# Optimization experiments

Hardware: AMD Instinct MI355X
Metric: run time of the kernel (lower is better)

The kernel has to match this reference:

```python
import jax, jax.numpy as jnp
import numpy as np

B, S, D, H = 2, 48, 256, 8
DH = D // H  # depth per head = 32
N = S * S    # flattened pair sequence length = 2304


def setup_inputs() -> dict:
    key = jax.random.key(0)
    ks = jax.random.split(key, 9)
    std = 1.0 / np.sqrt(D)
    x = jax.random.normal(ks[0], (B, S, S, D), dtype=jnp.float32)
    Wq = jax.random.normal(ks[1], (D, D), dtype=jnp.float32) * std
    Wk = jax.random.normal(ks[2], (D, D), dtype=jnp.float32) * std
    Wv = jax.random.normal(ks[3], (D, D), dtype=jnp.float32) * std
    Wo = jax.random.normal(ks[4], (D, D), dtype=jnp.float32) * std
    bq = jnp.zeros((D,), jnp.float32)
    bk = jnp.zeros((D,), jnp.float32)
    bv = jnp.zeros((D,), jnp.float32)
    bo = jnp.zeros((D,), jnp.float32)
    return {"pair_representation": x, "Wq": Wq, "bq": bq, "Wk": Wk, "bk": bk,
            "Wv": Wv, "bv": bv, "Wo": Wo, "bo": bo}


def reference(pair_representation, Wq, bq, Wk, bk, Wv, bv, Wo, bo):
    x = pair_representation.reshape(B, N, D)  # flatten (S,S) -> N

    def heads(t):  # (B,N,D) -> (B,H,N,DH)
        return t.reshape(B, N, H, DH).transpose(0, 2, 1, 3)

    q = heads(x @ Wq + bq)
    k = heads(x @ Wk + bk)
    v = heads(x @ Wv + bv)

    scale = 1.0 / jnp.sqrt(jnp.asarray(DH, jnp.float32))
    logits = jnp.einsum('bhnd,bhmd->bhnm', q, k) * scale  # (B,H,N,N)
    attn = jax.nn.softmax(logits, axis=-1)
    ctx = jnp.einsum('bhnm,bhmd->bhnd', attn, v)
    ctx = ctx.transpose(0, 2, 1, 3).reshape(B, N, D)
    return ctx @ Wo + bo  # (B, N, D)
```

## Files before the change

kernel.cpp:

```cpp
#include <hip/hip_runtime.h>
#include <math.h>

#define B 2
#define S 48
#define D 256
#define H 8
#define DH 32
#define N (S*S)
#define BN (B*N)
#define BH (B*H)
#define KS 4
#define KPZ (N/KS)
#define NE ((size_t)BN*D)
#define BHN (BH*N)

typedef _Float16 half8 __attribute__((ext_vector_type(8)));
typedef _Float16 half4_t __attribute__((ext_vector_type(4)));
typedef unsigned short ushort8_t __attribute__((ext_vector_type(8)));
typedef float floatx4 __attribute__((ext_vector_type(4)));

__device__ __forceinline__ void split8(const float* v, half8* hi, half8* lo) {
    #pragma unroll
    for (int j = 0; j < 8; j++) {
        _Float16 h = (_Float16)v[j];
        (*hi)[j] = h;
        (*lo)[j] = (_Float16)(v[j] - (float)h);
    }
}

__global__ __launch_bounds__(256) void convert_w(
    const float* __restrict__ Wq, const float* __restrict__ Wk,
    const float* __restrict__ Wv, const float* __restrict__ Wo,
    _Float16* __restrict__ wqh, _Float16* __restrict__ wql,
    _Float16* __restrict__ wkh, _Float16* __restrict__ wkl,
    _Float16* __restrict__ wvh, _Float16* __restrict__ wvl,
    _Float16* __restrict__ woh, _Float16* __restrict__ wol)
{
    const int t = threadIdx.x;
    const int z = blockIdx.y;
    const int tr = blockIdx.x >> 2, tc = blockIdx.x & 3;
    const float* W = (z == 0) ? Wq : (z == 1) ? Wk : (z == 2) ? Wv : Wo;
    _Float16* oh   = (z == 0) ? wqh : (z == 1) ? wkh : (z == 2) ? wvh : woh;
    _Float16* ol   = (z == 0) ? wql : (z == 1) ? wkl : (z == 2) ? wvl : wol;

    __shared__ float Ws[64 * 68];
    #pragma unroll
    for (int i = 0; i < 4; i++) {
        int idx = i * 1024 + t * 4;
        int r = idx >> 6, c = idx & 63;
        *(float4*)(&Ws[r * 68 + c]) =
            *(const float4*)(W + (size_t)(tr * 64 + r) * D + tc * 64 + c);
    }
    __syncthreads();
    #pragma unroll
    for (int it = 0; it < 2; it++) {
        int idx = it * 256 + t;
        int cc = idx & 63, k0 = (idx >> 6) * 8;
        float v[8];
        #pragma unroll
        for (int j = 0; j < 8; j++) v[j] = Ws[(k0 + j) * 68 + cc];
        half8 hi, lo;
        split8(v, &hi, &lo);
        size_t ob = (size_t)(tc * 64 + cc) * D + tr * 64 + k0;
        *(half8*)(oh + ob) = hi;
        *(half8*)(ol + ob) = lo;
    }
}

__global__ __launch_bounds__(256) void proj_gemm(
    const float* __restrict__ x,
    const _Float16* __restrict__ wqh, const _Float16* __restrict__ wql,
    const _Float16* __restrict__ wkh, const _Float16* __restrict__ wkl,
    const _Float16* __restrict__ wvh, const _Float16* __restrict__ wvl,
    const float* __restrict__ bq, const float* __restrict__ bk,
    const float* __restrict__ bv,
    _Float16* __restrict__ qh_o, _Float16* __restrict__ ql_o,
    _Float16* __restrict__ kh_o, _Float16* __restrict__ kl_o,
    _Float16* __restrict__ vh_o)
{
    __shared__ __align__(16) _Float16 AhS[64 * 72];
    __shared__ __align__(16) _Float16 AlS[64 * 72];
    __shared__ __align__(16) _Float16 BhS[64 * 72];
    __shared__ __align__(16) _Float16 BlS[64 * 72];

    const int z = blockIdx.z;
    const _Float16* bth = (z == 0) ? wqh : (z == 1) ? wkh : wvh;
    const _Float16* btl = (z == 0) ? wql : (z == 1) ? wkl : wvl;
    const float* bias   = (z == 0) ? bq : (z == 1) ? bk : bv;
    _Float16* oh        = (z == 0) ? qh_o : (z == 1) ? kh_o : vh_o;
    _Float16* ol        = (z == 0) ? ql_o : kl_o;
    const float scale   = (z == 0) ? rsqrtf((float)DH) * 1.44269504f : 1.0f;

    const int t = threadIdx.x;
    const int wv2 = t >> 6, lane = t & 63, l15 = lane & 15, quad = lane >> 4;
    const int rowbase = blockIdx.x * 64;
    const int colbase = blockIdx.y * 64;
    floatx4 acc[4] = {{0,0,0,0},{0,0,0,0},{0,0,0,0},{0,0,0,0}};

    for (int kb = 0; kb < D; kb += 64) {
        __syncthreads();
        #pragma unroll
        for (int i = 0; i < 2; i++) {
            int idx = i * 2048 + t * 8;
            int r = idx >> 6, c = idx & 63;
            const float* xp = x + (size_t)(rowbase + r) * D + kb + c;
            float4 x0 = *(const float4*)xp;
            float4 x1 = *(const float4*)(xp + 4);
            float v[8] = {x0.x, x0.y, x0.z, x0.w, x1.x, x1.y, x1.z, x1.w};
            half8 hi, lo;
            split8(v, &hi, &lo);
            *(half8*)(AhS + r * 72 + c) = hi;
            *(half8*)(AlS + r * 72 + c) = lo;
            *(ushort8_t*)(BhS + r * 72 + c) =
                *(const ushort8_t*)(bth + (size_t)(colbase + r) * D + kb + c);
            *(ushort8_t*)(BlS + r * 72 + c) =
                *(const ushort8_t*)(btl + (size_t)(colbase + r) * D + kb + c);
        }
        __syncthreads();
        #pragma unroll
        for (int ksx = 0; ksx < 2; ksx++) {
            half8 ah = *(const half8*)(AhS + (wv2 * 16 + l15) * 72 + ksx * 32 + quad * 8);
            half8 al = *(const half8*)(AlS + (wv2 * 16 + l15) * 72 + ksx * 32 + quad * 8);
            #pragma unroll
            for (int cg = 0; cg < 4; cg++) {
                half8 bh8 = *(const half8*)(BhS + (cg * 16 + l15) * 72 + ksx * 32 + quad * 8);
                half8 bl8 = *(const half8*)(BlS + (cg * 16 + l15) * 72 + ksx * 32 + quad * 8);
                acc[cg] = __builtin_amdgcn_mfma_f32_16x16x32_f16(ah, bh8, acc[cg], 0, 0, 0);
                acc[cg] = __builtin_amdgcn_mfma_f32_16x16x32_f16(al, bh8, acc[cg], 0, 0, 0);
                acc[cg] = __builtin_amdgcn_mfma_f32_16x16x32_f16(ah, bl8, acc[cg], 0, 0, 0);
            }
        }
    }

    const int bb = (rowbase >= N) ? 1 : 0;
    #pragma unroll
    for (int cg = 0; cg < 4; cg++) {
        int col = colbase + cg * 16 + l15;
        int hh = col >> 5, dh = col & 31;
        float bs = bias[col];
        #pragma unroll
        for (int r = 0; r < 4; r++) {
            int n = rowbase + wv2 * 16 + quad * 4 + r - bb * N;
            float v = (acc[cg][r] + bs) * scale;
            size_t ob = ((size_t)(bb * H + hh) * N + n) * DH + dh;
            _Float16 hi = (_Float16)v;
            oh[ob] = hi;
            if (z < 2) ol[ob] = (_Float16)(v - (float)hi);
        }
    }
}

__global__ __launch_bounds__(256) void attn_kernel(
    const _Float16* __restrict__ qh, const _Float16* __restrict__ ql,
    const _Float16* __restrict__ kh, const _Float16* __restrict__ kl,
    const _Float16* __restrict__ vh,
    float* __restrict__ ctx_part, float* __restrict__ lpart)
{
    __shared__ __align__(16) _Float16 Kh[64 * 40];
    __shared__ __align__(16) _Float16 Kl[64 * 40];
    __shared__ __align__(16) _Float16 Vt[32 * 72];

    const int t = threadIdx.x;
    const int wv2 = t >> 6, lane = t & 63, l15 = lane & 15, quad = lane >> 4;
    const int bh = blockIdx.y, kz = blockIdx.z;
    const int qbase = blockIdx.x * 128 + wv2 * 32;

    half4_t bqh[2][2], bql[2][2];
    #pragma unroll
    for (int qg = 0; qg < 2; qg++) {
        const size_t qoff = ((size_t)bh * N + qbase + qg * 16 + l15) * DH + quad * 4;
        bqh[qg][0] = *(const half4_t*)(qh + qoff);
        bqh[qg][1] = *(const half4_t*)(qh + qoff + 16);
        bql[qg][0] = *(const half4_t*)(ql + qoff);
        bql[qg][1] = *(const half4_t*)(ql + qoff + 16);
    }

    floatx4 acc[2][2] = {{{0,0,0,0},{0,0,0,0}},{{0,0,0,0},{0,0,0,0}}};
    float lsum[2] = {0.f, 0.f};

    const _Float16* kh_g = kh + (size_t)bh * N * DH;
    const _Float16* kl_g = kl + (size_t)bh * N * DH;
    const _Float16* vh_g = vh + (size_t)bh * N * DH;

    const int skey = t >> 2;
    const int sd0  = (t & 3) * 8;
    const int srot = 2 * (t & 3);

    for (int it = 0; it < KPZ / 64; it++) {
        const int key0 = kz * KPZ + it * 64;
        __syncthreads();
        {
            const size_t g = (size_t)key0 * DH + t * 8;
            ushort8_t kv = *(const ushort8_t*)(kh_g + g);
            ushort8_t lv = *(const ushort8_t*)(kl_g + g);
            ushort8_t vv = *(const ushort8_t*)(vh_g + g);
            *(ushort8_t*)(Kh + skey * 40 + sd0) = kv;
            *(ushort8_t*)(Kl + skey * 40 + sd0) = lv;
            unsigned short* vt = (unsigned short*)Vt;
            #pragma unroll
            for (int j = 0; j < 8; j++) {
                int jj = (j + srot) & 7;
                vt[(sd0 + jj) * 72 + skey] = vv[jj];
            }
        }
        __syncthreads();

        #pragma unroll
        for (int kg = 0; kg < 4; kg++) {
            const _Float16* kr = Kh + (kg * 16 + l15) * 40 + quad * 4;
            const _Float16* lr = Kl + (kg * 16 + l15) * 40 + quad * 4;
            half4_t ah0 = *(const half4_t*)(kr);
            half4_t ah1 = *(const half4_t*)(kr + 16);
            half4_t al0 = *(const half4_t*)(lr);
            half4_t al1 = *(const half4_t*)(lr + 16);
            half4_t va0 = *(const half4_t*)(Vt + l15 * 72 + kg * 16 + quad * 4);
            half4_t va1 = *(const half4_t*)(Vt + (16 + l15) * 72 + kg * 16 + quad * 4);
            #pragma unroll
            for (int qg = 0; qg < 2; qg++) {
                floatx4 s = {0, 0, 0, 0};
                s = __builtin_amdgcn_mfma_f32_16x16x16f16(ah0, bqh[qg][0], s, 0, 0, 0);
                s = __builtin_amdgcn_mfma_f32_16x16x16f16(al0, bqh[qg][0], s, 0, 0, 0);
                s = __builtin_amdgcn_mfma_f32_16x16x16f16(ah0, bql[qg][0], s, 0, 0, 0);
                s = __builtin_amdgcn_mfma_f32_16x16x16f16(ah1, bqh[qg][1], s, 0, 0, 0);
                s = __builtin_amdgcn_mfma_f32_16x16x16f16(al1, bqh[qg][1], s, 0, 0, 0);
                s = __builtin_amdgcn_mfma_f32_16x16x16f16(ah1, bql[qg][1], s, 0, 0, 0);
                float p0 = exp2f(s[0]), p1 = exp2f(s[1]);
                float p2 = exp2f(s[2]), p3 = exp2f(s[3]);
                lsum[qg] += (p0 + p1) + (p2 + p3);
                half4_t pf;
                pf[0] = (_Float16)p0; pf[1] = (_Float16)p1;
                pf[2] = (_Float16)p2; pf[3] = (_Float16)p3;
                acc[qg][0] = __builtin_amdgcn_mfma_f32_16x16x16f16(va0, pf, acc[qg][0], 0, 0, 0);
                acc[qg][1] = __builtin_amdgcn_mfma_f32_16x16x16f16(va1, pf, acc[qg][1], 0, 0, 0);
            }
        }
    }

    const int bb = bh / H, hh = bh % H;
    float* cp = ctx_part + (size_t)kz * NE;
    float* lp = lpart + (size_t)kz * BHN;
    #pragma unroll
    for (int qg = 0; qg < 2; qg++) {
        float ls = lsum[qg];
        ls += __shfl_xor(ls, 16);
        ls += __shfl_xor(ls, 32);
        int q = qbase + qg * 16 + l15;
        if (quad == 0) lp[bh * N + q] = ls;
        float* crow = cp + ((size_t)bb * N + q) * D + hh * DH;
        #pragma unroll
        for (int dg = 0; dg < 2; dg++)
            #pragma unroll
            for (int r = 0; r < 4; r++)
                crow[dg * 16 + quad * 4 + r] = acc[qg][dg][r];
    }
}

__global__ __launch_bounds__(256) void outproj_gemm(
    const float* __restrict__ ctx_part, const float* __restrict__ lpart,
    const _Float16* __restrict__ woh, const _Float16* __restrict__ wol,
    const float* __restrict__ bo, float* __restrict__ out)
{
    __shared__ __align__(16) _Float16 AhS[64 * 72];
    __shared__ __align__(16) _Float16 AlS[64 * 72];
    __shared__ __align__(16) _Float16 BhS[64 * 72];
    __shared__ __align__(16) _Float16 BlS[64 * 72];

    const int t = threadIdx.x;
    const int wv2 = t >> 6, lane = t & 63, l15 = lane & 15, quad = lane >> 4;
    const int rowbase = blockIdx.x * 64;
    const int colbase = blockIdx.y * 64;
    floatx4 acc[4] = {{0,0,0,0},{0,0,0,0},{0,0,0,0},{0,0,0,0}};

    for (int kb = 0; kb < D; kb += 64) {
        __syncthreads();
        #pragma unroll
        for (int i = 0; i < 2; i++) {
            int idx = i * 2048 + t * 8;
            int r = idx >> 6, c = idx & 63;
            int row = rowbase + r;
            int kcol = kb + c;
            int bb = (row >= N) ? 1 : 0;
            int n = row - bb * N;
            int bhn = (bb * H + (kcol >> 5)) * N + n;
            float ls = lpart[bhn] + lpart[BHN + bhn]
                     + lpart[2 * BHN + bhn] + lpart[3 * BHN + bhn];
            float inv = 1.0f / ls;
            const float* pp = ctx_part + (size_t)row * D + kcol;
            float4 a0 = *(const float4*)(pp),          a1 = *(const float4*)(pp + 4);
            float4 b0 = *(const float4*)(pp + NE),     b1 = *(const float4*)(pp + NE + 4);
            float4 c0 = *(const float4*)(pp + 2 * NE), c1 = *(const float4*)(pp + 2 * NE + 4);
            float4 d0 = *(const float4*)(pp + 3 * NE), d1 = *(const float4*)(pp + 3 * NE + 4);
            float v[8] = {(a0.x + b0.x + c0.x + d0.x) * inv,
                          (a0.y + b0.y + c0.y + d0.y) * inv,
                          (a0.z + b0.z + c0.z + d0.z) * inv,
                          (a0.w + b0.w + c0.w + d0.w) * inv,
                          (a1.x + b1.x + c1.x + d1.x) * inv,
                          (a1.y + b1.y + c1.y + d1.y) * inv,
                          (a1.z + b1.z + c1.z + d1.z) * inv,
                          (a1.w + b1.w + c1.w + d1.w) * inv};
            half8 hi, lo;
            split8(v, &hi, &lo);
            *(half8*)(AhS + r * 72 + c) = hi;
            *(half8*)(AlS + r * 72 + c) = lo;
            *(ushort8_t*)(BhS + r * 72 + c) =
                *(const ushort8_t*)(woh + (size_t)(colbase + r) * D + kb + c);
            *(ushort8_t*)(BlS + r * 72 + c) =
                *(const ushort8_t*)(wol + (size_t)(colbase + r) * D + kb + c);
        }
        __syncthreads();
        #pragma unroll
        for (int ksx = 0; ksx < 2; ksx++) {
            half8 ah = *(const half8*)(AhS + (wv2 * 16 + l15) * 72 + ksx * 32 + quad * 8);
            half8 al = *(const half8*)(AlS + (wv2 * 16 + l15) * 72 + ksx * 32 + quad * 8);
            #pragma unroll
            for (int cg = 0; cg < 4; cg++) {
                half8 bh8 = *(const half8*)(BhS + (cg * 16 + l15) * 72 + ksx * 32 + quad * 8);
                half8 bl8 = *(const half8*)(BlS + (cg * 16 + l15) * 72 + ksx * 32 + quad * 8);
                acc[cg] = __builtin_amdgcn_mfma_f32_16x16x32_f16(ah, bh8, acc[cg], 0, 0, 0);
                acc[cg] = __builtin_amdgcn_mfma_f32_16x16x32_f16(al, bh8, acc[cg], 0, 0, 0);
                acc[cg] = __builtin_amdgcn_mfma_f32_16x16x32_f16(ah, bl8, acc[cg], 0, 0, 0);
            }
        }
    }

    #pragma unroll
    for (int cg = 0; cg < 4; cg++) {
        int col = colbase + cg * 16 + l15;
        float bs = bo[col];
        #pragma unroll
        for (int r = 0; r < 4; r++) {
            int row = rowbase + wv2 * 16 + quad * 4 + r;
            out[(size_t)row * D + col] = acc[cg][r] + bs;
        }
    }
}

extern "C" void kernel_launch(void* const* d_in, const int* in_sizes, int n_in,
                              void* d_out, int out_size, void* d_ws, size_t ws_size,
                              hipStream_t stream)
{
    const float* x  = (const float*)d_in[0];
    const float* Wq = (const float*)d_in[1];
    const float* bq = (const float*)d_in[2];
    const float* Wk = (const float*)d_in[3];
    const float* bk = (const float*)d_in[4];
    const float* Wv = (const float*)d_in[5];
    const float* bv = (const float*)d_in[6];
    const float* Wo = (const float*)d_in[7];
    const float* bo = (const float*)d_in[8];
    float* out = (float*)d_out;

    const size_t WE = (size_t)D * D;

    float* ctx_part = (float*)d_ws;
    float* lpart    = ctx_part + (size_t)KS * NE;
    _Float16* qh  = (_Float16*)(lpart + (size_t)KS * BHN);
    _Float16* ql  = qh + NE;
    _Float16* kh  = ql + NE;
    _Float16* kl  = kh + NE;
    _Float16* vh  = kl + NE;
    _Float16* wqh = vh + NE;
    _Float16* wql = wqh + WE;
    _Float16* wkh = wql + WE;
    _Float16* wkl = wkh + WE;
    _Float16* wvh = wkl + WE;
    _Float16* wvl = wvh + WE;
    _Float16* woh = wvl + WE;
    _Float16* wol = woh + WE;

    convert_w<<<dim3(16, 4), 256, 0, stream>>>(
        Wq, Wk, Wv, Wo, wqh, wql, wkh, wkl, wvh, wvl, woh, wol);

    proj_gemm<<<dim3(BN / 64, D / 64, 3), 256, 0, stream>>>(
        x, wqh, wql, wkh, wkl, wvh, wvl, bq, bk, bv,
        qh, ql, kh, kl, vh);

    attn_kernel<<<dim3(N / 128, BH, KS), 256, 0, stream>>>(
        qh, ql, kh, kl, vh, ctx_part, lpart);

    outproj_gemm<<<dim3(BN / 64, D / 64), 256, 0, stream>>>(
        ctx_part, lpart, woh, wol, bo, out);
}
```

Before: 156.4 us.

## Use single fp16 QK, pre-transposed V, fuse weight split, raise key splits

Attention now computes Q·K^T with one fp16 MFMA (16x16x32) instead of a three-term hi/lo compensated product, and Q/K are stored only as fp16. The projection kernel writes V already transposed, so the attention kernel loads it into shared memory with plain vector copies instead of a scalar scatter. The separate weight-conversion kernel is removed; the GEMMs read fp32 weights and split them into hi/lo while loading tiles. The key dimension is split six ways instead of four for more parallelism, at the cost of more partial-sum traffic and lower logit precision.

```diff
diff --git a/kernel.cpp b/kernel.cpp
--- a/kernel.cpp
+++ b/kernel.cpp
@@ -9,7 +9,7 @@
 #define N (S*S)
 #define BN (B*N)
 #define BH (B*H)
-#define KS 4
+#define KS 6
 #define KPZ (N/KS)
 #define NE ((size_t)BN*D)
 #define BHN (BH*N)
@@ -28,55 +28,13 @@
     }
 }
 
-__global__ __launch_bounds__(256) void convert_w(
-    const float* __restrict__ Wq, const float* __restrict__ Wk,
-    const float* __restrict__ Wv, const float* __restrict__ Wo,
-    _Float16* __restrict__ wqh, _Float16* __restrict__ wql,
-    _Float16* __restrict__ wkh, _Float16* __restrict__ wkl,
-    _Float16* __restrict__ wvh, _Float16* __restrict__ wvl,
-    _Float16* __restrict__ woh, _Float16* __restrict__ wol)
-{
-    const int t = threadIdx.x;
-    const int z = blockIdx.y;
-    const int tr = blockIdx.x >> 2, tc = blockIdx.x & 3;
-    const float* W = (z == 0) ? Wq : (z == 1) ? Wk : (z == 2) ? Wv : Wo;
-    _Float16* oh   = (z == 0) ? wqh : (z == 1) ? wkh : (z == 2) ? wvh : woh;
-    _Float16* ol   = (z == 0) ? wql : (z == 1) ? wkl : (z == 2) ? wvl : wol;
-
-    __shared__ float Ws[64 * 68];
-    #pragma unroll
-    for (int i = 0; i < 4; i++) {
-        int idx = i * 1024 + t * 4;
-        int r = idx >> 6, c = idx & 63;
-        *(float4*)(&Ws[r * 68 + c]) =
-            *(const float4*)(W + (size_t)(tr * 64 + r) * D + tc * 64 + c);
-    }
-    __syncthreads();
-    #pragma unroll
-    for (int it = 0; it < 2; it++) {
-        int idx = it * 256 + t;
-        int cc = idx & 63, k0 = (idx >> 6) * 8;
-        float v[8];
-        #pragma unroll
-        for (int j = 0; j < 8; j++) v[j] = Ws[(k0 + j) * 68 + cc];
-        half8 hi, lo;
-        split8(v, &hi, &lo);
-        size_t ob = (size_t)(tc * 64 + cc) * D + tr * 64 + k0;
-        *(half8*)(oh + ob) = hi;
-        *(half8*)(ol + ob) = lo;
-    }
-}
-
-__global__ __launch_bounds__(256) void proj_gemm(
+__global__ __launch_bounds__(256) void proj_kernel(
     const float* __restrict__ x,
-    const _Float16* __restrict__ wqh, const _Float16* __restrict__ wql,
-    const _Float16* __restrict__ wkh, const _Float16* __restrict__ wkl,
-    const _Float16* __restrict__ wvh, const _Float16* __restrict__ wvl,
-    const float* __restrict__ bq, const float* __restrict__ bk,
-    const float* __restrict__ bv,
-    _Float16* __restrict__ qh_o, _Float16* __restrict__ ql_o,
-    _Float16* __restrict__ kh_o, _Float16* __restrict__ kl_o,
-    _Float16* __restrict__ vh_o)
+    const float* __restrict__ Wq, const float* __restrict__ bq,
+    const float* __restrict__ Wk, const float* __restrict__ bk,
+    const float* __restrict__ Wv, const float* __restrict__ bv,
+    _Float16* __restrict__ qbuf, _Float16* __restrict__ kbuf,
+    _Float16* __restrict__ vtbuf)
 {
     __shared__ __align__(16) _Float16 AhS[64 * 72];
     __shared__ __align__(16) _Float16 AlS[64 * 72];
@@ -84,26 +42,23 @@
     __shared__ __align__(16) _Float16 BlS[64 * 72];
 
     const int z = blockIdx.z;
-    const _Float16* bth = (z == 0) ? wqh : (z == 1) ? wkh : wvh;
-    const _Float16* btl = (z == 0) ? wql : (z == 1) ? wkl : wvl;
-    const float* bias   = (z == 0) ? bq : (z == 1) ? bk : bv;
-    _Float16* oh        = (z == 0) ? qh_o : (z == 1) ? kh_o : vh_o;
-    _Float16* ol        = (z == 0) ? ql_o : kl_o;
-    const float scale   = (z == 0) ? rsqrtf((float)DH) * 1.44269504f : 1.0f;
+    const float* W    = (z == 0) ? Wq : (z == 1) ? Wk : Wv;
+    const float* bias = (z == 0) ? bq : (z == 1) ? bk : bv;
+    const float scale = (z == 0) ? rsqrtf((float)DH) * 1.44269504f : 1.0f;
 
     const int t = threadIdx.x;
     const int wv2 = t >> 6, lane = t & 63, l15 = lane & 15, quad = lane >> 4;
-    const int rowbase = blockIdx.x * 64;
-    const int colbase = blockIdx.y * 64;
+    const int rowb = blockIdx.x * 64;
+    const int colb = blockIdx.y * 64;
     floatx4 acc[4] = {{0,0,0,0},{0,0,0,0},{0,0,0,0},{0,0,0,0}};
 
-    for (int kb = 0; kb < D; kb += 64) {
+    for (int kb0 = 0; kb0 < D; kb0 += 64) {
         __syncthreads();
         #pragma unroll
         for (int i = 0; i < 2; i++) {
             int idx = i * 2048 + t * 8;
             int r = idx >> 6, c = idx & 63;
-            const float* xp = x + (size_t)(rowbase + r) * D + kb + c;
+            const float* xp = x + (size_t)(rowb + r) * D + kb0 + c;
             float4 x0 = *(const float4*)xp;
             float4 x1 = *(const float4*)(xp + 4);
             float v[8] = {x0.x, x0.y, x0.z, x0.w, x1.x, x1.y, x1.z, x1.w};
@@ -111,10 +66,19 @@
             split8(v, &hi, &lo);
             *(half8*)(AhS + r * 72 + c) = hi;
             *(half8*)(AlS + r * 72 + c) = lo;
-            *(ushort8_t*)(BhS + r * 72 + c) =
-                *(const ushort8_t*)(bth + (size_t)(colbase + r) * D + kb + c);
-            *(ushort8_t*)(BlS + r * 72 + c) =
-                *(const ushort8_t*)(btl + (size_t)(colbase + r) * D + kb + c);
+        }
+        #pragma unroll
+        for (int i = 0; i < 2; i++) {
+            int u = i * 256 + t;
+            int cc = u & 63, k0 = (u >> 6) * 8;
+            float v[8];
+            #pragma unroll
+            for (int j = 0; j < 8; j++)
+                v[j] = W[(size_t)(kb0 + k0 + j) * D + colb + cc];
+            half8 hi, lo;
+            split8(v, &hi, &lo);
+            *(half8*)(BhS + cc * 72 + k0) = hi;
+            *(half8*)(BlS + cc * 72 + k0) = lo;
         }
         __syncthreads();
         #pragma unroll
@@ -132,32 +96,36 @@
         }
     }
 
-    const int bb = (rowbase >= N) ? 1 : 0;
+    const int bb = (rowb >= N) ? 1 : 0;
     #pragma unroll
     for (int cg = 0; cg < 4; cg++) {
-        int col = colbase + cg * 16 + l15;
+        int col = colb + cg * 16 + l15;
         int hh = col >> 5, dh = col & 31;
         float bs = bias[col];
-        #pragma unroll
-        for (int r = 0; r < 4; r++) {
-            int n = rowbase + wv2 * 16 + quad * 4 + r - bb * N;
-            float v = (acc[cg][r] + bs) * scale;
-            size_t ob = ((size_t)(bb * H + hh) * N + n) * DH + dh;
-            _Float16 hi = (_Float16)v;
-            oh[ob] = hi;
-            if (z < 2) ol[ob] = (_Float16)(v - (float)hi);
+        if (z < 2) {
+            _Float16* op = (z == 0) ? qbuf : kbuf;
+            #pragma unroll
+            for (int r = 0; r < 4; r++) {
+                int n = rowb + wv2 * 16 + quad * 4 + r - bb * N;
+                float v = (acc[cg][r] + bs) * scale;
+                op[((size_t)(bb * H + hh) * N + n) * DH + dh] = (_Float16)v;
+            }
+        } else {
+            int n0 = rowb + wv2 * 16 + quad * 4 - bb * N;
+            half4_t pk;
+            #pragma unroll
+            for (int r = 0; r < 4; r++) pk[r] = (_Float16)(acc[cg][r] + bs);
+            *(half4_t*)(vtbuf + ((size_t)(bb * H + hh) * DH + dh) * N + n0) = pk;
         }
     }
 }
 
 __global__ __launch_bounds__(256) void attn_kernel(
-    const _Float16* __restrict__ qh, const _Float16* __restrict__ ql,
-    const _Float16* __restrict__ kh, const _Float16* __restrict__ kl,
-    const _Float16* __restrict__ vh,
+    const _Float16* __restrict__ qbuf, const _Float16* __restrict__ kbuf,
+    const _Float16* __restrict__ vtbuf,
     float* __restrict__ ctx_part, float* __restrict__ lpart)
 {
-    __shared__ __align__(16) _Float16 Kh[64 * 40];
-    __shared__ __align__(16) _Float16 Kl[64 * 40];
+    __shared__ __align__(16) _Float16 Ks[64 * 40];
     __shared__ __align__(16) _Float16 Vt[32 * 72];
 
     const int t = threadIdx.x;
@@ -165,100 +133,67 @@
     const int bh = blockIdx.y, kz = blockIdx.z;
     const int qbase = blockIdx.x * 128 + wv2 * 32;
 
-    half4_t bqh[2][2], bql[2][2];
-    #pragma unroll
-    for (int qg = 0; qg < 2; qg++) {
-        const size_t qoff = ((size_t)bh * N + qbase + qg * 16 + l15) * DH + quad * 4;
-        bqh[qg][0] = *(const half4_t*)(qh + qoff);
-        bqh[qg][1] = *(const half4_t*)(qh + qoff + 16);
-        bql[qg][0] = *(const half4_t*)(ql + qoff);
-        bql[qg][1] = *(const half4_t*)(ql + qoff + 16);
-    }
+    half8 bq8[2];
+    #pragma unroll
+    for (int qg = 0; qg < 2; qg++)
+        bq8[qg] = *(const half8*)(qbuf +
+            ((size_t)bh * N + qbase + qg * 16 + l15) * DH + quad * 8);
 
     floatx4 acc[2][2] = {{{0,0,0,0},{0,0,0,0}},{{0,0,0,0},{0,0,0,0}}};
     float lsum[2] = {0.f, 0.f};
 
-    const _Float16* kh_g = kh + (size_t)bh * N * DH;
-    const _Float16* kl_g = kl + (size_t)bh * N * DH;
-    const _Float16* vh_g = vh + (size_t)bh * N * DH;
-
-    const int skey = t >> 2;
-    const int sd0  = (t & 3) * 8;
-    const int srot = 2 * (t & 3);
+    const int skey = t >> 2, sd0 = (t & 3) * 8;
+    const int svd = t >> 3, svk = (t & 7) * 8;
 
     for (int it = 0; it < KPZ / 64; it++) {
         const int key0 = kz * KPZ + it * 64;
         __syncthreads();
-        {
-            const size_t g = (size_t)key0 * DH + t * 8;
-            ushort8_t kv = *(const ushort8_t*)(kh_g + g);
-            ushort8_t lv = *(const ushort8_t*)(kl_g + g);
-            ushort8_t vv = *(const ushort8_t*)(vh_g + g);
-            *(ushort8_t*)(Kh + skey * 40 + sd0) = kv;
-            *(ushort8_t*)(Kl + skey * 40 + sd0) = lv;
-            unsigned short* vt = (unsigned short*)Vt;
-            #pragma unroll
-            for (int j = 0; j < 8; j++) {
-                int jj = (j + srot) & 7;
-                vt[(sd0 + jj) * 72 + skey] = vv[jj];
-            }
-        }
+        *(ushort8_t*)(Ks + skey * 40 + sd0) =
+            *(const ushort8_t*)(kbuf + ((size_t)bh * N + key0 + skey) * DH + sd0);
+        *(ushort8_t*)(Vt + svd * 72 + svk) =
+            *(const ushort8_t*)(vtbuf + ((size_t)bh * DH + svd) * N + key0 + svk);
         __syncthreads();
 
         #pragma unroll
         for (int kg = 0; kg < 4; kg++) {
-            const _Float16* kr = Kh + (kg * 16 + l15) * 40 + quad * 4;
-            const _Float16* lr = Kl + (kg * 16 + l15) * 40 + quad * 4;
-            half4_t ah0 = *(const half4_t*)(kr);
-            half4_t ah1 = *(const half4_t*)(kr + 16);
-            half4_t al0 = *(const half4_t*)(lr);
-            half4_t al1 = *(const half4_t*)(lr + 16);
+            half8 ka = *(const half8*)(Ks + (kg * 16 + l15) * 40 + quad * 8);
             half4_t va0 = *(const half4_t*)(Vt + l15 * 72 + kg * 16 + quad * 4);
             half4_t va1 = *(const half4_t*)(Vt + (16 + l15) * 72 + kg * 16 + quad * 4);
             #pragma unroll
             for (int qg = 0; qg < 2; qg++) {
                 floatx4 s = {0, 0, 0, 0};
-                s = __builtin_amdgcn_mfma_f32_16x16x16f16(ah0, bqh[qg][0], s, 0, 0, 0);
-                s = __builtin_amdgcn_mfma_f32_16x16x16f16(al0, bqh[qg][0], s, 0, 0, 0);
-                s = __builtin_amdgcn_mfma_f32_16x16x16f16(ah0, bql[qg][0], s, 0, 0, 0);
-                s = __builtin_amdgcn_mfma_f32_16x16x16f16(ah1, bqh[qg][1], s, 0, 0, 0);
-                s = __builtin_amdgcn_mfma_f32_16x16x16f16(al1, bqh[qg][1], s, 0, 0, 0);
-                s = __builtin_amdgcn_mfma_f32_16x16x16f16(ah1, bql[qg][1], s, 0, 0, 0);
-                float p0 = exp2f(s[0]), p1 = exp2f(s[1]);
-                float p2 = exp2f(s[2]), p3 = exp2f(s[3]);
-                lsum[qg] += (p0 + p1) + (p2 + p3);
+                s = __builtin_amdgcn_mfma_f32_16x16x32_f16(ka, bq8[qg], s, 0, 0, 0);
                 half4_t pf;
-                pf[0] = (_Float16)p0; pf[1] = (_Float16)p1;
-                pf[2] = (_Float16)p2; pf[3] = (_Float16)p3;
+                #pragma unroll
+                for (int r = 0; r < 4; r++) {
+                    float p = exp2f(s[r]);
+                    lsum[qg] += p;
+                    pf[r] = (_Float16)p;
+                }
                 acc[qg][0] = __builtin_amdgcn_mfma_f32_16x16x16f16(va0, pf, acc[qg][0], 0, 0, 0);
                 acc[qg][1] = __builtin_amdgcn_mfma_f32_16x16x16f16(va1, pf, acc[qg][1], 0, 0, 0);
             }
         }
     }
 
-    const int bb = bh / H, hh = bh % H;
-    float* cp = ctx_part + (size_t)kz * NE;
-    float* lp = lpart + (size_t)kz * BHN;
+    const int bb = bh >> 3, hh = bh & 7;
     #pragma unroll
     for (int qg = 0; qg < 2; qg++) {
         float ls = lsum[qg];
         ls += __shfl_xor(ls, 16);
         ls += __shfl_xor(ls, 32);
         int q = qbase + qg * 16 + l15;
-        if (quad == 0) lp[bh * N + q] = ls;
-        float* crow = cp + ((size_t)bb * N + q) * D + hh * DH;
-        #pragma unroll
-        for (int dg = 0; dg < 2; dg++)
-            #pragma unroll
-            for (int r = 0; r < 4; r++)
-                crow[dg * 16 + quad * 4 + r] = acc[qg][dg][r];
-    }
-}
-
-__global__ __launch_bounds__(256) void outproj_gemm(
+        if (quad == 0) lpart[(size_t)kz * BHN + bh * N + q] = ls;
+        float* crow = ctx_part + (size_t)kz * NE + ((size_t)bb * N + q) * D + hh * DH;
+        *(floatx4*)(crow + quad * 4)      = acc[qg][0];
+        *(floatx4*)(crow + 16 + quad * 4) = acc[qg][1];
+    }
+}
+
+__global__ __launch_bounds__(256) void outproj_kernel(
     const float* __restrict__ ctx_part, const float* __restrict__ lpart,
-    const _Float16* __restrict__ woh, const _Float16* __restrict__ wol,
-    const float* __restrict__ bo, float* __restrict__ out)
+    const float* __restrict__ Wo, const float* __restrict__ bo,
+    float* __restrict__ out)
 {
     __shared__ __align__(16) _Float16 AhS[64 * 72];
     __shared__ __align__(16) _Float16 AlS[64 * 72];
@@ -267,45 +202,53 @@
 
     const int t = threadIdx.x;
     const int wv2 = t >> 6, lane = t & 63, l15 = lane & 15, quad = lane >> 4;
-    const int rowbase = blockIdx.x * 64;
-    const int colbase = blockIdx.y * 64;
+    const int rowb = blockIdx.x * 64;
+    const int colb = blockIdx.y * 64;
     floatx4 acc[4] = {{0,0,0,0},{0,0,0,0},{0,0,0,0},{0,0,0,0}};
 
-    for (int kb = 0; kb < D; kb += 64) {
+    for (int kb0 = 0; kb0 < D; kb0 += 64) {
         __syncthreads();
         #pragma unroll
         for (int i = 0; i < 2; i++) {
             int idx = i * 2048 + t * 8;
             int r = idx >> 6, c = idx & 63;
-            int row = rowbase + r;
-            int kcol = kb + c;
+            int row = rowb + r;
+            int kcol = kb0 + c;
             int bb = (row >= N) ? 1 : 0;
             int n = row - bb * N;
             int bhn = (bb * H + (kcol >> 5)) * N + n;
-            float ls = lpart[bhn] + lpart[BHN + bhn]
-                     + lpart[2 * BHN + bhn] + lpart[3 * BHN + bhn];
+            float ls = 0.f;
+            #pragma unroll
+            for (int zz = 0; zz < KS; zz++) ls += lpart[(size_t)zz * BHN + bhn];
             float inv = 1.0f / ls;
-            const float* pp = ctx_part + (size_t)row * D + kcol;
-            float4 a0 = *(const float4*)(pp),          a1 = *(const float4*)(pp + 4);
-            float4 b0 = *(const float4*)(pp + NE),     b1 = *(const float4*)(pp + NE + 4);
-            float4 c0 = *(const float4*)(pp + 2 * NE), c1 = *(const float4*)(pp + 2 * NE + 4);
-            float4 d0 = *(const float4*)(pp + 3 * NE), d1 = *(const float4*)(pp + 3 * NE + 4);
-            float v[8] = {(a0.x + b0.x + c0.x + d0.x) * inv,
-                          (a0.y + b0.y + c0.y + d0.y) * inv,
-                          (a0.z + b0.z + c0.z + d0.z) * inv,
-                          (a0.w + b0.w + c0.w + d0.w) * inv,
-                          (a1.x + b1.x + c1.x + d1.x) * inv,
-                          (a1.y + b1.y + c1.y + d1.y) * inv,
-                          (a1.z + b1.z + c1.z + d1.z) * inv,
-                          (a1.w + b1.w + c1.w + d1.w) * inv};
+            float v[8] = {};
+            #pragma unroll
+            for (int zz = 0; zz < KS; zz++) {
+                const float* pp = ctx_part + (size_t)zz * NE + (size_t)row * D + kcol;
+                float4 p0 = *(const float4*)pp;
+                float4 p1 = *(const float4*)(pp + 4);
+                v[0] += p0.x; v[1] += p0.y; v[2] += p0.z; v[3] += p0.w;
+                v[4] += p1.x; v[5] += p1.y; v[6] += p1.z; v[7] += p1.w;
+            }
+            #pragma unroll
+            for (int j = 0; j < 8; j++) v[j] *= inv;
             half8 hi, lo;
             split8(v, &hi, &lo);
             *(half8*)(AhS + r * 72 + c) = hi;
             *(half8*)(AlS + r * 72 + c) = lo;
-            *(ushort8_t*)(BhS + r * 72 + c) =
-                *(const ushort8_t*)(woh + (size_t)(colbase + r) * D + kb + c);
-            *(ushort8_t*)(BlS + r * 72 + c) =
-                *(const ushort8_t*)(wol + (size_t)(colbase + r) * D + kb + c);
+        }
+        #pragma unroll
+        for (int i = 0; i < 2; i++) {
+            int u = i * 256 + t;
+            int cc = u & 63, k0 = (u >> 6) * 8;
+            float v[8];
+            #pragma unroll
+            for (int j = 0; j < 8; j++)
+                v[j] = Wo[(size_t)(kb0 + k0 + j) * D + colb + cc];
+            half8 hi, lo;
+            split8(v, &hi, &lo);
+            *(half8*)(BhS + cc * 72 + k0) = hi;
+            *(half8*)(BlS + cc * 72 + k0) = lo;
         }
         __syncthreads();
         #pragma unroll
@@ -325,11 +268,11 @@
 
     #pragma unroll
     for (int cg = 0; cg < 4; cg++) {
-        int col = colbase + cg * 16 + l15;
+        int col = colb + cg * 16 + l15;
         float bs = bo[col];
         #pragma unroll
         for (int r = 0; r < 4; r++) {
-            int row = rowbase + wv2 * 16 + quad * 4 + r;
+            int row = rowb + wv2 * 16 + quad * 4 + r;
             out[(size_t)row * D + col] = acc[cg][r] + bs;
         }
     }
@@ -350,34 +293,18 @@
     const float* bo = (const float*)d_in[8];
     float* out = (float*)d_out;
 
-    const size_t WE = (size_t)D * D;
-
     float* ctx_part = (float*)d_ws;
     float* lpart    = ctx_part + (size_t)KS * NE;
-    _Float16* qh  = (_Float16*)(lpart + (size_t)KS * BHN);
-    _Float16* ql  = qh + NE;
-    _Float16* kh  = ql + NE;
-    _Float16* kl  = kh + NE;
-    _Float16* vh  = kl + NE;
-    _Float16* wqh = vh + NE;
-    _Float16* wql = wqh + WE;
-    _Float16* wkh = wql + WE;
-    _Float16* wkl = wkh + WE;
-    _Float16* wvh = wkl + WE;
-    _Float16* wvl = wvh + WE;
-    _Float16* woh = wvl + WE;
-    _Float16* wol = woh + WE;
-
-    convert_w<<<dim3(16, 4), 256, 0, stream>>>(
-        Wq, Wk, Wv, Wo, wqh, wql, wkh, wkl, wvh, wvl, woh, wol);
-
-    proj_gemm<<<dim3(BN / 64, D / 64, 3), 256, 0, stream>>>(
-        x, wqh, wql, wkh, wkl, wvh, wvl, bq, bk, bv,
-        qh, ql, kh, kl, vh);
+    _Float16* qbuf  = (_Float16*)(lpart + (size_t)KS * BHN);
+    _Float16* kbuf  = qbuf + NE;
+    _Float16* vtbuf = kbuf + NE;
+
+    proj_kernel<<<dim3(BN / 64, D / 64, 3), 256, 0, stream>>>(
+        x, Wq, bq, Wk, bk, Wv, bv, qbuf, kbuf, vtbuf);
 
     attn_kernel<<<dim3(N / 128, BH, KS), 256, 0, stream>>>(
-        qh, ql, kh, kl, vh, ctx_part, lpart);
-
-    outproj_gemm<<<dim3(BN / 64, D / 64), 256, 0, stream>>>(
-        ctx_part, lpart, woh, wol, bo, out);
-}
+        qbuf, kbuf, vtbuf, ctx_part, lpart);
+
+    outproj_kernel<<<dim3(BN / 64, D / 64), 256, 0, stream>>>(
+        ctx_part, lpart, Wo, bo, out);
+}
```

New measurement: 146.3 us. 6.5% less time.
